# Kernel tuning notes

Measured on AMD Instinct MI355X. Metric: run time of the kernel, lower is better.

The kernel has to match this reference:

```python
import jax, jax.numpy as jnp
import numpy as np

B, N, H, S, NSEC = 1, 8192, 256, 128, 8
TAU = 0.5
DEPTH_LO, DEPTH_HI = 0.0, 2.4
PADDING = 0.1
EPS = 1e-6
_p = float(np.clip(TAU, 1e-4, 1.0 - 1e-4))
LOGIT_TAU = float(np.log(_p / (1.0 - _p)))


def mlp(p, W1, b1, W2, b2, W3, b3, W4, b4):
    # p: [..., 3] -> logit [...]
    h = jax.nn.softplus(p @ W1 + b1)
    h = jax.nn.softplus(h @ W2 + b2)
    h = jax.nn.softplus(h @ W3 + b3)
    return (h @ W4 + b4)[..., 0]


def cube_intersection(ray0, rd):
    # Faithful port of check_ray_intersection_with_unit_cube.
    p_dist = 0.5 + PADDING / 2.0
    plane = jnp.concatenate([jnp.full((3,), p_dist), jnp.full((3,), -p_dist)])  # (6,)
    nom = plane - jnp.tile(ray0, (1, 1, 2))          # (B,N,6)
    den = jnp.tile(rd, (1, 1, 2))
    den = jnp.where(jnp.abs(den) < 1e-9, 1e-9, den)  # numerical guard
    d_int = nom / den                                 # (B,N,6)
    p_int = ray0[:, :, None, :] + d_int[..., None] * rd[:, :, None, :]  # (B,N,6,3)
    inside = jnp.all(jnp.abs(p_int) <= p_dist + EPS, axis=-1)           # (B,N,6)
    mask = inside.sum(-1) == 2                                           # rays hitting cube
    # pick the (exactly two) intersecting planes in ascending plane order,
    # matching torch boolean indexing semantics
    plane_id = jnp.arange(6)
    key = jnp.where(inside, plane_id, plane_id + 6)
    idx2 = jnp.argsort(key, axis=-1)[..., :2]                            # (B,N,2)
    p2 = jnp.take_along_axis(p_int, idx2[..., None], axis=2)            # (B,N,2,3)
    norm_rd = jnp.linalg.norm(rd, axis=-1)                               # (B,N)
    d2 = jnp.linalg.norm(p2 - ray0[:, :, None, :], axis=-1) / norm_rd[..., None]
    d2 = jnp.where(mask[..., None], d2, 0.0)
    d2 = jnp.sort(d2, axis=-1)
    return d2, mask


def _secant(d_low, f_low, d_high, f_high):
    den = f_high - f_low
    den = jnp.where(jnp.abs(den) < 1e-12, 1e-12, den)
    return -f_low * (d_high - d_low) / den + d_low


def reference(ray0, ray_direction, W1, b1, W2, b2, W3, b3, W4, b4):
    rd = ray_direction
    dec = lambda p: mlp(p, W1, b1, W2, b2, W3, b3, W4, b4)
    sg = jax.lax.stop_gradient

    # ---- proposal depths (no grad, as torch no_grad ray-marching) ----
    t = jnp.linspace(0.0, 1.0, S)                       # (S,)
    d_default = DEPTH_LO + t * (DEPTH_HI - DEPTH_LO)
    d2, mask_cube = cube_intersection(ray0, rd)
    d_cube = d2[..., 0:1] + t * (d2[..., 1:2] - d2[..., 0:1])   # (B,N,S)
    d_prop = jnp.where(mask_cube[..., None], d_cube, d_default)
    d_prop = sg(d_prop)

    p_prop = sg(ray0)[:, :, None, :] + d_prop[..., None] * sg(rd)[:, :, None, :]
    val = sg(dec(p_prop)) - LOGIT_TAU                   # (B,N,S)

    mask_0_not_occupied = val[..., 0] < 0
    sign_matrix = jnp.concatenate(
        [jnp.sign(val[..., :-1] * val[..., 1:]), jnp.ones(val.shape[:-1] + (1,), val.dtype)], -1)
    cost = sign_matrix * jnp.arange(S, 0, -1, dtype=val.dtype)
    idx = jnp.argmin(cost, -1)                          # first sign-change step
    vmin = jnp.min(cost, -1)
    f_low = jnp.take_along_axis(val, idx[..., None], -1)[..., 0]
    mask = (vmin < 0) & (f_low < 0) & mask_0_not_occupied

    idx_hi = jnp.minimum(idx + 1, S - 1)
    d_low = jnp.take_along_axis(d_prop, idx[..., None], -1)[..., 0]
    d_high = jnp.take_along_axis(d_prop, idx_hi[..., None], -1)[..., 0]
    f_high = jnp.take_along_axis(val, idx_hi[..., None], -1)[..., 0]

    # ---- secant refinement (no grad in torch) ----
    r0s, rds = sg(ray0), sg(rd)
    d_pred = _secant(d_low, f_low, d_high, f_high)
    for _ in range(NSEC):
        f_mid = sg(dec(r0s + d_pred[..., None] * rds)) - LOGIT_TAU
        low = f_mid < 0
        d_low = jnp.where(low, d_pred, d_low)
        f_low = jnp.where(low, f_mid, f_low)
        d_high = jnp.where(low, d_high, d_pred)
        f_high = jnp.where(low, f_high, f_mid)
        d_pred = _secant(d_low, f_low, d_high, f_high)

    # ---- differentiable implicit-gradient correction (analytic backward of
    # DepthFunction: dd/dtheta = -(df/dtheta)/(df/dd) at the surface point) ----
    d_star = sg(d_pred)
    f_of_d = lambda d: dec(ray0 + d[..., None] * rd) - LOGIT_TAU
    f_val = f_of_d(d_star)                              # differentiable wrt params/rays
    _, df_dd = jax.jvp(f_of_d, (d_star,), (jnp.ones_like(d_star),))
    df_dd = sg(df_dd)
    df_dd = jnp.where(jnp.abs(df_dd) < 1e-6,
                      jnp.where(df_dd < 0, -1e-6, 1e-6), df_dd)
    d_out = d_star - f_val / df_dd
    d_final = jnp.where(mask, d_out, 0.0)
    return d_final


def setup_inputs() -> dict:
    key = jax.random.key(0)
    ks = jax.random.split(key, 10)
    origin = jnp.array([0.0, 0.0, -1.5])
    ray0 = origin + 0.01 * jax.random.normal(ks[0], (B, N, 3), dtype=jnp.float32)
    target = jax.random.uniform(ks[1], (B, N, 3), minval=-0.4, maxval=0.4, dtype=jnp.float32)
    rd = target - ray0
    rd = rd / jnp.linalg.norm(rd, axis=-1, keepdims=True)
    W1 = jax.random.normal(ks[2], (3, H), dtype=jnp.float32) / jnp.sqrt(3.0)
    b1 = 0.1 * jax.random.normal(ks[3], (H,), dtype=jnp.float32)
    W2 = jax.random.normal(ks[4], (H, H), dtype=jnp.float32) / jnp.sqrt(float(H))
    b2 = 0.1 * jax.random.normal(ks[5], (H,), dtype=jnp.float32)
    W3 = jax.random.normal(ks[6], (H, H), dtype=jnp.float32) / jnp.sqrt(float(H))
    b3 = 0.1 * jax.random.normal(ks[7], (H,), dtype=jnp.float32)
    W4 = jax.random.normal(ks[8], (H, 1), dtype=jnp.float32) / jnp.sqrt(float(H))
    b4 = 0.1 * jax.random.normal(ks[9], (1,), dtype=jnp.float32)
    return {"ray0": ray0, "ray_direction": rd, "W1": W1, "b1": b1,
            "W2": W2, "b2": b2, "W3": W3, "b3": b3, "W4": W4, "b4": b4}
```

## Files before the change

kernel.cpp:

```cpp
#include <hip/hip_runtime.h>
#include <math.h>

#define NRAY 8192
#define SSAMP 128
#define HD 256
#define AROW 264
#define A1ROW 40
#define FIXCAP 262144
#define FIXTHR 0.018f

typedef short s16x8 __attribute__((ext_vector_type(8)));
typedef float f32x4 __attribute__((ext_vector_type(4)));

__device__ __forceinline__ unsigned short f2bf(float f) {
    unsigned u = __float_as_uint(f);
    u += 0x7fffu + ((u >> 16) & 1u);
    return (unsigned short)(u >> 16);
}
__device__ __forceinline__ float bf2f(unsigned short s) {
    return __uint_as_float(((unsigned)s) << 16);
}
__device__ __forceinline__ void split2(float f, unsigned short& hi, unsigned short& lo) {
    unsigned u = __float_as_uint(f);
    hi = (unsigned short)(u >> 16);
    float r = f - __uint_as_float(u & 0xFFFF0000u);
    lo = f2bf(r);
}
__device__ __forceinline__ unsigned pack_bf16x2(float a, float b) {
    unsigned r;
    asm("v_cvt_pk_bf16_f32 %0, %1, %2" : "=v"(r) : "v"(a), "v"(b));
    return r;
}
__device__ __forceinline__ float softplus_fast(float x) {
    return fmaxf(x, 0.0f) + __logf(1.0f + __expf(-fabsf(x)));
}
__device__ __forceinline__ float softplus_cheap(float x) {
    float m = __expf(-fabsf(x));
    float p = fmaf(m, fmaf(0.14258f, m, -0.44943f), 1.0f);
    return fmaxf(x, 0.0f) + m * p;
}
__device__ __forceinline__ float sigmoid_fast(float x) {
    return 1.0f / (1.0f + __expf(-x));
}

__global__ __launch_bounds__(256)
void prep_kernel(const float* __restrict__ W1, const float* __restrict__ b1,
                 const float* __restrict__ W2, const float* __restrict__ W3,
                 const float* __restrict__ ray0, const float* __restrict__ rdg,
                 unsigned short* __restrict__ P2, unsigned short* __restrict__ P3,
                 unsigned short* __restrict__ B1, float* __restrict__ rayinfo,
                 int* __restrict__ fix_cnt) {
    const int b = blockIdx.x, tid = threadIdx.x;
    if (b < 256) {
        int idx = b * 256 + tid;
        int k = idx >> 8, n = idx & 255;
        int nt = n >> 4, kt = k >> 5, lq = (k >> 3) & 3, j = k & 7;
        int lane = (lq << 4) | (n & 15);
        size_t off = (size_t)((nt * 8 + kt) * 2) * 512 + (size_t)lane * 8 + j;
        float w = W2[idx];
        unsigned short hi = f2bf(w);
        P2[off] = hi; P2[off + 512] = f2bf(w - bf2f(hi));
        w = W3[idx];
        hi = f2bf(w);
        P3[off] = hi; P3[off + 512] = f2bf(w - bf2f(hi));
    } else if (b < 288) {
        int idx = (b - 256) * 256 + tid;
        int w = idx & 511;
        int lane = w >> 3, j = w & 7;
        int k = ((lane >> 4) << 3) + j;
        int n = ((idx >> 9) << 4) + (lane & 15);
        unsigned short s = 0;
        if (k < 3) s = f2bf(W1[k * HD + n]);
        else if (k == 3) s = f2bf(b1[n]);
        else if (k < 7) s = f2bf(W1[(k - 4) * HD + n]);
        else if (k == 7) { unsigned short bh = f2bf(b1[n]); s = f2bf(b1[n] - bf2f(bh)); }
        else if (k < 11) { float wv = W1[(k - 8) * HD + n]; unsigned short wh = f2bf(wv); s = f2bf(wv - bf2f(wh)); }
        B1[idx] = s;
    } else {
        int r = (b - 288) * 256 + tid;
        if (r == 0) *fix_cnt = 0;
        float o0 = ray0[3 * r], o1 = ray0[3 * r + 1], o2 = ray0[3 * r + 2];
        float v0 = rdg[3 * r], v1 = rdg[3 * r + 1], v2 = rdg[3 * r + 2];
        const float pd = 0.55f, lim = pd + 1e-6f;
        float di[6]; int insk[6]; int cnt = 0;
        for (int k = 0; k < 6; k++) {
            int a = k % 3;
            float pl = (k < 3) ? pd : -pd;
            float den = (a == 0) ? v0 : ((a == 1) ? v1 : v2);
            if (fabsf(den) < 1e-9f) den = 1e-9f;
            float oa = (a == 0) ? o0 : ((a == 1) ? o1 : o2);
            float dd = (pl - oa) / den;
            float px = o0 + dd * v0, py = o1 + dd * v1, pz = o2 + dd * v2;
            int ins = (fabsf(px) <= lim) && (fabsf(py) <= lim) && (fabsf(pz) <= lim);
            di[k] = dd; insk[k] = ins; cnt += ins;
        }
        float d0 = 0.f, sl = 2.4f;
        if (cnt == 2) {
            int k1 = -1, k2 = -1;
            for (int k = 0; k < 6; k++) if (insk[k]) { if (k1 < 0) k1 = k; else k2 = k; }
            float nrd = sqrtf(v0 * v0 + v1 * v1 + v2 * v2);
            float ax = di[k1] * v0, ay = di[k1] * v1, az = di[k1] * v2;
            float d1n = sqrtf(ax * ax + ay * ay + az * az) / nrd;
            float bx = di[k2] * v0, by = di[k2] * v1, bz = di[k2] * v2;
            float d2n = sqrtf(bx * bx + by * by + bz * bz) / nrd;
            d0 = fminf(d1n, d2n);
            sl = fmaxf(d1n, d2n) - d0;
        }
        float* ri = rayinfo + (size_t)r * 8;
        ri[0] = d0; ri[1] = sl;
        ri[2] = o0; ri[3] = o1; ri[4] = o2;
        ri[5] = v0; ri[6] = v1; ri[7] = v2;
    }
}


template<int MT, int NT>
__device__ __forceinline__ void gemm_l1(const unsigned short* A1,
                                        const unsigned short* __restrict__ B1,
                                        f32x4 acc[MT][NT], int lane, int ntbase) {
    const int r15 = lane & 15, q = lane >> 4;
    s16x8 wh[NT];
#pragma unroll
    for (int nt = 0; nt < NT; nt++)
        wh[nt] = *(((const s16x8*)B1) + (size_t)(ntbase + nt) * 64 + lane);
#pragma unroll
    for (int mt = 0; mt < MT; mt++) {
        s16x8 ah = *(const s16x8*)(A1 + (mt * 16 + r15) * A1ROW + q * 8);
#pragma unroll
        for (int nt = 0; nt < NT; nt++)
            acc[mt][nt] = __builtin_amdgcn_mfma_f32_16x16x32_bf16(wh[nt], ah, (f32x4){0.f,0.f,0.f,0.f}, 0, 0, 0);
    }
}

template<int MT, int NT>
__device__ __forceinline__ void gemm_1t(const unsigned short* Act,
                                        const unsigned short* __restrict__ Wp,
                                        f32x4 acc[MT][NT], int lane, int ntbase) {
#pragma unroll
    for (int mt = 0; mt < MT; mt++)
#pragma unroll
        for (int nt = 0; nt < NT; nt++) acc[mt][nt] = (f32x4){0.f, 0.f, 0.f, 0.f};
    const int r15 = lane & 15, q = lane >> 4;
#pragma unroll 2
    for (int kt = 0; kt < 8; kt++) {
        s16x8 wh[NT];
#pragma unroll
        for (int nt = 0; nt < NT; nt++) {
            const s16x8* wp = ((const s16x8*)Wp) + (size_t)((ntbase + nt) * 8 + kt) * 128 + lane;
            wh[nt] = wp[0];
        }
        const int kc = kt * 32 + q * 8;
#pragma unroll
        for (int mt = 0; mt < MT; mt++) {
            s16x8 ah = *(const s16x8*)(Act + (mt * 16 + r15) * AROW + kc);
#pragma unroll
            for (int nt = 0; nt < NT; nt++)
                acc[mt][nt] = __builtin_amdgcn_mfma_f32_16x16x32_bf16(wh[nt], ah, acc[mt][nt], 0, 0, 0);
        }
    }
}

template<int MT, int NT>
__device__ __forceinline__ void gemm_3t(const unsigned short* Ahi, const unsigned short* Alo,
                                        const unsigned short* __restrict__ Wp,
                                        f32x4 acc[MT][NT], int lane, int ntbase) {
#pragma unroll
    for (int mt = 0; mt < MT; mt++)
#pragma unroll
        for (int nt = 0; nt < NT; nt++) acc[mt][nt] = (f32x4){0.f, 0.f, 0.f, 0.f};
    const int r15 = lane & 15, q = lane >> 4;
#pragma unroll 2
    for (int kt = 0; kt < 8; kt++) {
        s16x8 wh[NT], wl[NT];
#pragma unroll
        for (int nt = 0; nt < NT; nt++) {
            const s16x8* wp = ((const s16x8*)Wp) + (size_t)((ntbase + nt) * 8 + kt) * 128 + lane;
            wh[nt] = wp[0];
            wl[nt] = wp[64];
        }
        const int kc = kt * 32 + q * 8;
#pragma unroll
        for (int mt = 0; mt < MT; mt++) {
            s16x8 ah = *(const s16x8*)(Ahi + (mt * 16 + r15) * AROW + kc);
            s16x8 al = *(const s16x8*)(Alo + (mt * 16 + r15) * AROW + kc);
#pragma unroll
            for (int nt = 0; nt < NT; nt++) {
                acc[mt][nt] = __builtin_amdgcn_mfma_f32_16x16x32_bf16(wh[nt], ah, acc[mt][nt], 0, 0, 0);
                acc[mt][nt] = __builtin_amdgcn_mfma_f32_16x16x32_bf16(wl[nt], ah, acc[mt][nt], 0, 0, 0);
                acc[mt][nt] = __builtin_amdgcn_mfma_f32_16x16x32_bf16(wh[nt], al, acc[mt][nt], 0, 0, 0);
            }
        }
    }
}

template<int MT, int NT>
__device__ __forceinline__ void gemm_dual(const unsigned short* Avh, const unsigned short* Avl,
                                          const unsigned short* Ath, const unsigned short* Atl,
                                          const unsigned short* __restrict__ Wp,
                                          f32x4 av[MT][NT], f32x4 at[MT][NT], int lane, int ntbase) {
#pragma unroll
    for (int mt = 0; mt < MT; mt++)
#pragma unroll
        for (int nt = 0; nt < NT; nt++) {
            av[mt][nt] = (f32x4){0.f, 0.f, 0.f, 0.f};
            at[mt][nt] = (f32x4){0.f, 0.f, 0.f, 0.f};
        }
    const int r15 = lane & 15, q = lane >> 4;
#pragma unroll 2
    for (int kt = 0; kt < 8; kt++) {
        s16x8 wh[NT], wl[NT];
#pragma unroll
        for (int nt = 0; nt < NT; nt++) {
            const s16x8* wp = ((const s16x8*)Wp) + (size_t)((ntbase + nt) * 8 + kt) * 128 + lane;
            wh[nt] = wp[0];
            wl[nt] = wp[64];
        }
        const int kc = kt * 32 + q * 8;
#pragma unroll
        for (int mt = 0; mt < MT; mt++) {
            s16x8 avhf = *(const s16x8*)(Avh + (mt * 16 + r15) * AROW + kc);
            s16x8 avlf = *(const s16x8*)(Avl + (mt * 16 + r15) * AROW + kc);
            s16x8 athf = *(const s16x8*)(Ath + (mt * 16 + r15) * AROW + kc);
            s16x8 atlf = *(const s16x8*)(Atl + (mt * 16 + r15) * AROW + kc);
#pragma unroll
            for (int nt = 0; nt < NT; nt++) {
                av[mt][nt] = __builtin_amdgcn_mfma_f32_16x16x32_bf16(wh[nt], avhf, av[mt][nt], 0, 0, 0);
                av[mt][nt] = __builtin_amdgcn_mfma_f32_16x16x32_bf16(wl[nt], avhf, av[mt][nt], 0, 0, 0);
                av[mt][nt] = __builtin_amdgcn_mfma_f32_16x16x32_bf16(wh[nt], avlf, av[mt][nt], 0, 0, 0);
                at[mt][nt] = __builtin_amdgcn_mfma_f32_16x16x32_bf16(wh[nt], athf, at[mt][nt], 0, 0, 0);
                at[mt][nt] = __builtin_amdgcn_mfma_f32_16x16x32_bf16(wl[nt], athf, at[mt][nt], 0, 0, 0);
                at[mt][nt] = __builtin_amdgcn_mfma_f32_16x16x32_bf16(wh[nt], atlf, at[mt][nt], 0, 0, 0);
            }
        }
    }
}

template<int MT, int NT>
__device__ __forceinline__ void epi_l1(f32x4 acc[MT][NT], unsigned short* Ahi, int lane, int wn0) {
    const int r15 = lane & 15, q = lane >> 4;
#pragma unroll
    for (int mt = 0; mt < MT; mt++) {
        unsigned short* rowp = Ahi + (mt * 16 + r15) * AROW + wn0 + q * 4;
#pragma unroll
        for (int nt = 0; nt < NT; nt++) {
            float h0 = softplus_cheap(acc[mt][nt][0]);
            float h1 = softplus_cheap(acc[mt][nt][1]);
            float h2 = softplus_cheap(acc[mt][nt][2]);
            float h3 = softplus_cheap(acc[mt][nt][3]);
            *reinterpret_cast<uint2*>(rowp + nt * 16) =
                make_uint2(pack_bf16x2(h0, h1), pack_bf16x2(h2, h3));
        }
    }
}

template<int MT, int NT>
__device__ __forceinline__ void epi_l1_sp(f32x4 acc[MT][NT], unsigned short* Ahi, unsigned short* Alo,
                                          int lane, int wn0) {
    const int r15 = lane & 15, q = lane >> 4;
#pragma unroll
    for (int mt = 0; mt < MT; mt++) {
        const int rowoff = (mt * 16 + r15) * AROW + wn0 + q * 4;
#pragma unroll
        for (int nt = 0; nt < NT; nt++) {
            float h0 = softplus_fast(acc[mt][nt][0]);
            float h1 = softplus_fast(acc[mt][nt][1]);
            float h2 = softplus_fast(acc[mt][nt][2]);
            float h3 = softplus_fast(acc[mt][nt][3]);
            unsigned x0 = pack_bf16x2(h0, h1), x1 = pack_bf16x2(h2, h3);
            float l0 = h0 - __uint_as_float(x0 << 16);
            float l1 = h1 - __uint_as_float(x0 & 0xFFFF0000u);
            float l2 = h2 - __uint_as_float(x1 << 16);
            float l3 = h3 - __uint_as_float(x1 & 0xFFFF0000u);
            *reinterpret_cast<uint2*>(Ahi + rowoff + nt * 16) = make_uint2(x0, x1);
            *reinterpret_cast<uint2*>(Alo + rowoff + nt * 16) =
                make_uint2(pack_bf16x2(l0, l1), pack_bf16x2(l2, l3));
        }
    }
}

template<int MT, int NT>
__device__ __forceinline__ void epi_hidden_1t(f32x4 acc[MT][NT], const float* __restrict__ b,
                                              unsigned short* Ahi, int lane, int wn0) {
    const int r15 = lane & 15, q = lane >> 4;
    f32x4 bb[NT];
#pragma unroll
    for (int nt = 0; nt < NT; nt++) bb[nt] = *(const f32x4*)(b + wn0 + nt * 16 + q * 4);
#pragma unroll
    for (int mt = 0; mt < MT; mt++) {
        unsigned short* rowp = Ahi + (mt * 16 + r15) * AROW + wn0 + q * 4;
#pragma unroll
        for (int nt = 0; nt < NT; nt++) {
            float h0 = softplus_cheap(acc[mt][nt][0] + bb[nt][0]);
            float h1 = softplus_cheap(acc[mt][nt][1] + bb[nt][1]);
            float h2 = softplus_cheap(acc[mt][nt][2] + bb[nt][2]);
            float h3 = softplus_cheap(acc[mt][nt][3] + bb[nt][3]);
            *reinterpret_cast<uint2*>(rowp + nt * 16) =
                make_uint2(pack_bf16x2(h0, h1), pack_bf16x2(h2, h3));
        }
    }
}

template<int MT, int NT>
__device__ __forceinline__ void epi_hidden_sp(f32x4 acc[MT][NT], const float* __restrict__ b,
                                              unsigned short* Ahi, unsigned short* Alo,
                                              int lane, int wn0) {
    const int r15 = lane & 15, q = lane >> 4;
    f32x4 bb[NT];
#pragma unroll
    for (int nt = 0; nt < NT; nt++) bb[nt] = *(const f32x4*)(b + wn0 + nt * 16 + q * 4);
#pragma unroll
    for (int mt = 0; mt < MT; mt++) {
        const int rowoff = (mt * 16 + r15) * AROW + wn0 + q * 4;
#pragma unroll
        for (int nt = 0; nt < NT; nt++) {
            float h0 = softplus_fast(acc[mt][nt][0] + bb[nt][0]);
            float h1 = softplus_fast(acc[mt][nt][1] + bb[nt][1]);
            float h2 = softplus_fast(acc[mt][nt][2] + bb[nt][2]);
            float h3 = softplus_fast(acc[mt][nt][3] + bb[nt][3]);
            unsigned x0 = pack_bf16x2(h0, h1), x1 = pack_bf16x2(h2, h3);
            float l0 = h0 - __uint_as_float(x0 << 16);
            float l1 = h1 - __uint_as_float(x0 & 0xFFFF0000u);
            float l2 = h2 - __uint_as_float(x1 << 16);
            float l3 = h3 - __uint_as_float(x1 & 0xFFFF0000u);
            *reinterpret_cast<uint2*>(Ahi + rowoff + nt * 16) = make_uint2(x0, x1);
            *reinterpret_cast<uint2*>(Alo + rowoff + nt * 16) =
                make_uint2(pack_bf16x2(l0, l1), pack_bf16x2(l2, l3));
        }
    }
}

template<int MT, int NT>
__device__ __forceinline__ void epi_dual(f32x4 av[MT][NT], f32x4 at[MT][NT], const float* __restrict__ b,
                                         unsigned short* Avh, unsigned short* Avl,
                                         unsigned short* Ath, unsigned short* Atl,
                                         int lane, int wn0) {
    const int r15 = lane & 15, q = lane >> 4;
    f32x4 bb[NT];
#pragma unroll
    for (int nt = 0; nt < NT; nt++) bb[nt] = *(const f32x4*)(b + wn0 + nt * 16 + q * 4);
#pragma unroll
    for (int mt = 0; mt < MT; mt++) {
        const int rowoff = (mt * 16 + r15) * AROW + wn0 + q * 4;
#pragma unroll
        for (int nt = 0; nt < NT; nt++) {
            float h[4], g[4];
#pragma unroll
            for (int r = 0; r < 4; r++) {
                float z = av[mt][nt][r] + bb[nt][r];
                h[r] = softplus_fast(z);
                g[r] = sigmoid_fast(z) * at[mt][nt][r];
            }
            unsigned x0 = pack_bf16x2(h[0], h[1]), x1 = pack_bf16x2(h[2], h[3]);
            float l0 = h[0] - __uint_as_float(x0 << 16);
            float l1 = h[1] - __uint_as_float(x0 & 0xFFFF0000u);
            float l2 = h[2] - __uint_as_float(x1 << 16);
            float l3 = h[3] - __uint_as_float(x1 & 0xFFFF0000u);
            *reinterpret_cast<uint2*>(Avh + rowoff + nt * 16) = make_uint2(x0, x1);
            *reinterpret_cast<uint2*>(Avl + rowoff + nt * 16) =
                make_uint2(pack_bf16x2(l0, l1), pack_bf16x2(l2, l3));
            x0 = pack_bf16x2(g[0], g[1]); x1 = pack_bf16x2(g[2], g[3]);
            l0 = g[0] - __uint_as_float(x0 << 16);
            l1 = g[1] - __uint_as_float(x0 & 0xFFFF0000u);
            l2 = g[2] - __uint_as_float(x1 << 16);
            l3 = g[3] - __uint_as_float(x1 & 0xFFFF0000u);
            *reinterpret_cast<uint2*>(Ath + rowoff + nt * 16) = make_uint2(x0, x1);
            *reinterpret_cast<uint2*>(Atl + rowoff + nt * 16) =
                make_uint2(pack_bf16x2(l0, l1), pack_bf16x2(l2, l3));
        }
    }
}

template<int MT, int NT, bool CH>
__device__ __forceinline__ void l4_reduce(f32x4 acc[MT][NT], const float* __restrict__ b3,
                                          const float* __restrict__ W4,
                                          float* partial, int lane, int wn0) {
    const int r15 = lane & 15, q = lane >> 4;
    f32x4 w4v[NT], b3v[NT];
#pragma unroll
    for (int nt = 0; nt < NT; nt++) {
        w4v[nt] = *(const f32x4*)(W4 + wn0 + nt * 16 + q * 4);
        b3v[nt] = *(const f32x4*)(b3 + wn0 + nt * 16 + q * 4);
    }
#pragma unroll
    for (int mt = 0; mt < MT; mt++) {
        float p = 0.f;
#pragma unroll
        for (int nt = 0; nt < NT; nt++)
#pragma unroll
            for (int r = 0; r < 4; r++) {
                float z = acc[mt][nt][r] + b3v[nt][r];
                float h = CH ? softplus_cheap(z) : softplus_fast(z);
                p = fmaf(h, w4v[nt][r], p);
            }
        p += __shfl_xor(p, 16, 64);
        p += __shfl_xor(p, 32, 64);
        if (q == 0) partial[mt * 16 + r15] = p;
    }
}

template<int MT, int NT>
__device__ __forceinline__ void l4_reduce_dual(f32x4 av[MT][NT], f32x4 at[MT][NT],
                                               const float* __restrict__ b3, const float* __restrict__ W4,
                                               float* pv, float* pt, int lane, int wn0) {
    const int r15 = lane & 15, q = lane >> 4;
    f32x4 w4v[NT], b3v[NT];
#pragma unroll
    for (int nt = 0; nt < NT; nt++) {
        w4v[nt] = *(const f32x4*)(W4 + wn0 + nt * 16 + q * 4);
        b3v[nt] = *(const f32x4*)(b3 + wn0 + nt * 16 + q * 4);
    }
#pragma unroll
    for (int mt = 0; mt < MT; mt++) {
        float sv = 0.f, st = 0.f;
#pragma unroll
        for (int nt = 0; nt < NT; nt++)
#pragma unroll
            for (int r = 0; r < 4; r++) {
                float z = av[mt][nt][r] + b3v[nt][r];
                sv = fmaf(softplus_fast(z), w4v[nt][r], sv);
                st = fmaf(sigmoid_fast(z) * at[mt][nt][r], w4v[nt][r], st);
            }
        sv += __shfl_xor(sv, 16, 64);
        sv += __shfl_xor(sv, 32, 64);
        st += __shfl_xor(st, 16, 64);
        st += __shfl_xor(st, 32, 64);
        if (q == 0) {
            pv[mt * 16 + r15] = sv;
            pt[mt * 16 + r15] = st;
        }
    }
}

__global__ __launch_bounds__(512, 4)
void coarse_mfma(const float* __restrict__ rayinfo,
                 const unsigned short* __restrict__ B1,
                 const unsigned short* __restrict__ P2, const float* __restrict__ b2,
                 const unsigned short* __restrict__ P3, const float* __restrict__ b3,
                 const float* __restrict__ W4, const float* __restrict__ b4,
                 float* __restrict__ val_out, float* __restrict__ dprop_out,
                 int* __restrict__ fix_cnt, int* __restrict__ fix_list) {
    __shared__ __align__(16) unsigned short Ahi[128 * AROW];
    __shared__ __align__(16) unsigned short A1[128 * A1ROW];
    float* partial = (float*)A1;
    const int tid = threadIdx.x;
    const int lane = tid & 63, wave = tid >> 6;
    const int r = blockIdx.x;

    if (tid < 128) {
        const float* ri = rayinfo + (size_t)r * 8;
        const int s = tid;
        float t = (float)s * (1.0f / 127.0f);
        float d = fmaf(t, ri[1], ri[0]);
        dprop_out[r * SSAMP + s] = d;
        float px = fmaf(d, ri[5], ri[2]);
        float py = fmaf(d, ri[6], ri[3]);
        float pz = fmaf(d, ri[7], ri[4]);
        unsigned short hx, lx, hy, ly, hz, lz;
        split2(px, hx, lx); split2(py, hy, ly); split2(pz, hz, lz);
        unsigned short* row = A1 + tid * A1ROW;
        row[0] = hx; row[1] = hy; row[2] = hz; row[3] = 0x3F80u;
        row[4] = lx; row[5] = ly; row[6] = lz; row[7] = 0x3F80u;
        row[8] = hx; row[9] = hy; row[10] = hz;
#pragma unroll
        for (int c = 11; c < 32; c++) row[c] = 0;
    }
    __syncthreads();
    f32x4 acc[8][2];
    gemm_l1<8, 2>(A1, B1, acc, lane, wave * 2);
    epi_l1<8, 2>(acc, Ahi, lane, wave * 32);
    __syncthreads();
    gemm_1t<8, 2>(Ahi, P2, acc, lane, wave * 2);
    __syncthreads();
    epi_hidden_1t<8, 2>(acc, b2, Ahi, lane, wave * 32);
    __syncthreads();
    gemm_1t<8, 2>(Ahi, P3, acc, lane, wave * 2);
    l4_reduce<8, 2, true>(acc, b3, W4, &partial[wave * 128], lane, wave * 32);
    __syncthreads();
    if (tid < 128) {
        float v = b4[0];
#pragma unroll
        for (int w = 0; w < 8; w++) v += partial[w * 128 + tid];
        int idx = r * SSAMP + tid;
        val_out[idx] = v;
        if (fabsf(v) < FIXTHR) {
            int pos = atomicAdd(fix_cnt, 1);
            if (pos < FIXCAP) fix_list[pos] = idx;
        }
    }
}

__global__ __launch_bounds__(256, 4)
void fixup3_mfma(const int* __restrict__ counter, const int* __restrict__ list,
                 float* __restrict__ val, const float* __restrict__ dprop,
                 const float* __restrict__ ray0, const float* __restrict__ rdg,
                 const unsigned short* __restrict__ B1,
                 const unsigned short* __restrict__ P2, const float* __restrict__ b2,
                 const unsigned short* __restrict__ P3, const float* __restrict__ b3,
                 const float* __restrict__ W4, const float* __restrict__ b4) {
    __shared__ __align__(16) unsigned short Ahi[32 * AROW];
    __shared__ __align__(16) unsigned short Alo[32 * AROW];
    __shared__ __align__(16) unsigned short A1[32 * A1ROW];
    __shared__ float partial[4][32];
    __shared__ int bidxs[32];
    const int cnt = min(*counter, FIXCAP);
    const int base = blockIdx.x * 32;
    if (base >= cnt) return;
    const int tid = threadIdx.x;
    const int lane = tid & 63, wave = tid >> 6;
    if (tid < 32) {
        const int i = min(base + tid, cnt - 1);
        const int bidx = list[i];
        bidxs[tid] = bidx;
        const int rr = bidx >> 7;
        float d = dprop[bidx];
        float px = ray0[3 * rr] + d * rdg[3 * rr];
        float py = ray0[3 * rr + 1] + d * rdg[3 * rr + 1];
        float pz = ray0[3 * rr + 2] + d * rdg[3 * rr + 2];
        unsigned short hx, lx, hy, ly, hz, lz;
        split2(px, hx, lx); split2(py, hy, ly); split2(pz, hz, lz);
        unsigned short* row = A1 + tid * A1ROW;
        row[0] = hx; row[1] = hy; row[2] = hz; row[3] = 0x3F80u;
        row[4] = lx; row[5] = ly; row[6] = lz; row[7] = 0x3F80u;
        row[8] = hx; row[9] = hy; row[10] = hz;
#pragma unroll
        for (int c = 11; c < 32; c++) row[c] = 0;
    }
    __syncthreads();
    f32x4 acc[2][4];
    gemm_l1<2, 4>(A1, B1, acc, lane, wave * 4);
    epi_l1_sp<2, 4>(acc, Ahi, Alo, lane, wave * 64);
    __syncthreads();
    gemm_3t<2, 4>(Ahi, Alo, P2, acc, lane, wave * 4);
    __syncthreads();
    epi_hidden_sp<2, 4>(acc, b2, Ahi, Alo, lane, wave * 64);
    __syncthreads();
    gemm_3t<2, 4>(Ahi, Alo, P3, acc, lane, wave * 4);
    l4_reduce<2, 4, false>(acc, b3, W4, &partial[wave][0], lane, wave * 64);
    __syncthreads();
    if (tid < 32) {
        float v = partial[0][tid] + partial[1][tid] + partial[2][tid] + partial[3][tid] + b4[0];
        val[bidxs[tid]] = v;
    }
}

__global__ __launch_bounds__(256, 4)
void refine_mfma(const float* __restrict__ val, const float* __restrict__ dprop,
                 const float* __restrict__ ray0, const float* __restrict__ rdg,
                 const float* __restrict__ W1, const float* __restrict__ b1,
                 const unsigned short* __restrict__ P2, const float* __restrict__ b2,
                 const unsigned short* __restrict__ P3, const float* __restrict__ b3,
                 const float* __restrict__ W4, const float* __restrict__ b4,
                 float* __restrict__ out) {
    __shared__ __align__(16) unsigned short Avh[16 * AROW];
    __shared__ __align__(16) unsigned short Avl[16 * AROW];
    __shared__ __align__(16) unsigned short Ath[16 * AROW];
    __shared__ __align__(16) unsigned short Atl[16 * AROW];
    __shared__ float partial[4][16], ptan[4][16];
    __shared__ float dl[16], fl[16], dh[16], fh[16], dps[16];
    __shared__ int mks[16];
    unsigned short* Ahi = Avh;
    const int tid = threadIdx.x;
    const int lane = tid & 63, wave = tid >> 6;
    const int r0 = blockIdx.x * 16;

    for (int i = 0; i < 4; i++) {
        const int r = r0 + wave * 4 + i;
        const float2 v = *(const float2*)(val + (size_t)r * SSAMP + lane * 2);
        const float2 dd = *(const float2*)(dprop + (size_t)r * SSAMP + lane * 2);
        float vnext = __shfl_down(v.x, 1, 64);
        const int s0 = lane * 2, s1 = s0 + 1;
        float pr0 = v.x * v.y;
        int sg0 = (pr0 > 0.f) ? 1 : ((pr0 < 0.f) ? -1 : 0);
        int k0 = (sg0 * (SSAMP - s0) + 129) * 256 + s0;
        int k1;
        if (lane == 63) {
            k1 = (1 + 129) * 256 + 127;
        } else {
            float pr1 = v.y * vnext;
            int sg1 = (pr1 > 0.f) ? 1 : ((pr1 < 0.f) ? -1 : 0);
            k1 = (sg1 * (SSAMP - s1) + 129) * 256 + s1;
        }
        int k = min(k0, k1);
#pragma unroll
        for (int m = 1; m < 64; m <<= 1) k = min(k, __shfl_xor(k, m, 64));
        int bidx = k & 255;
        int cmin = (k >> 8) - 129;
        int idxh = min(bidx + 1, SSAMP - 1);
        int ow = bidx >> 1, oh = idxh >> 1;
        float fa = __shfl(v.x, ow, 64), fb = __shfl(v.y, ow, 64);
        float da = __shfl(dd.x, ow, 64), db = __shfl(dd.y, ow, 64);
        float fa2 = __shfl(v.x, oh, 64), fb2 = __shfl(v.y, oh, 64);
        float da2 = __shfl(dd.x, oh, 64), db2 = __shfl(dd.y, oh, 64);
        float v0 = __shfl(v.x, 0, 64);
        if (lane == 0) {
            float f_low = (bidx & 1) ? fb : fa;
            float d_low = (bidx & 1) ? db : da;
            float f_high = (idxh & 1) ? fb2 : fa2;
            float d_high = (idxh & 1) ? db2 : da2;
            int sl = wave * 4 + i;
            mks[sl] = (cmin < 0) && (f_low < 0.f) && (v0 < 0.f);
            float den = f_high - f_low;
            if (fabsf(den) < 1e-12f) den = 1e-12f;
            dl[sl] = d_low; fl[sl] = f_low; dh[sl] = d_high; fh[sl] = f_high;
            dps[sl] = -f_low * (d_high - d_low) / den + d_low;
        }
    }
    __syncthreads();
    for (int it = 0; it < 8; it++) {
        {
            const int pt = tid >> 4, jb = (tid & 15) << 4;
            const int rr = r0 + pt;
            float d = dps[pt];
            float px = ray0[3 * rr] + d * rdg[3 * rr];
            float py = ray0[3 * rr + 1] + d * rdg[3 * rr + 1];
            float pz = ray0[3 * rr + 2] + d * rdg[3 * rr + 2];
            for (int j = jb; j < jb + 16; j += 4) {
                float4 wa = *(const float4*)(W1 + j);
                float4 wb = *(const float4*)(W1 + 256 + j);
                float4 wc = *(const float4*)(W1 + 512 + j);
                float4 bb = *(const float4*)(b1 + j);
                float z[4];
                z[0] = fmaf(px, wa.x, fmaf(py, wb.x, fmaf(pz, wc.x, bb.x)));
                z[1] = fmaf(px, wa.y, fmaf(py, wb.y, fmaf(pz, wc.y, bb.y)));
                z[2] = fmaf(px, wa.z, fmaf(py, wb.z, fmaf(pz, wc.z, bb.z)));
                z[3] = fmaf(px, wa.w, fmaf(py, wb.w, fmaf(pz, wc.w, bb.w)));
                *reinterpret_cast<uint2*>(&Ahi[pt * AROW + j]) =
                    make_uint2(pack_bf16x2(softplus_cheap(z[0]), softplus_cheap(z[1])),
                               pack_bf16x2(softplus_cheap(z[2]), softplus_cheap(z[3])));
            }
        }
        __syncthreads();
        f32x4 acc[1][4];
        gemm_1t<1, 4>(Ahi, P2, acc, lane, wave * 4);
        __syncthreads();
        epi_hidden_1t<1, 4>(acc, b2, Ahi, lane, wave * 64);
        __syncthreads();
        gemm_1t<1, 4>(Ahi, P3, acc, lane, wave * 4);
        l4_reduce<1, 4, true>(acc, b3, W4, &partial[wave][0], lane, wave * 64);
        __syncthreads();
        if (tid < 16) {
            float fm = partial[0][tid] + partial[1][tid] + partial[2][tid] + partial[3][tid] + b4[0];
            float dpv = dps[tid];
            float dlv = dl[tid], flv = fl[tid], dhv = dh[tid], fhv = fh[tid];
            if (fm < 0.f) { dlv = dpv; flv = fm; } else { dhv = dpv; fhv = fm; }
            float den = fhv - flv;
            if (fabsf(den) < 1e-12f) den = 1e-12f;
            dps[tid] = -flv * (dhv - dlv) / den + dlv;
            dl[tid] = dlv; fl[tid] = flv; dh[tid] = dhv; fh[tid] = fhv;
        }
        __syncthreads();
    }
    {
        const int pt = tid >> 4, jb = (tid & 15) << 4;
        const int rr = r0 + pt;
        float d = dps[pt];
        float v0 = rdg[3 * rr], v1 = rdg[3 * rr + 1], v2 = rdg[3 * rr + 2];
        float px = ray0[3 * rr] + d * v0;
        float py = ray0[3 * rr + 1] + d * v1;
        float pz = ray0[3 * rr + 2] + d * v2;
        for (int j = jb; j < jb + 16; j += 4) {
            float4 wa = *(const float4*)(W1 + j);
            float4 wb = *(const float4*)(W1 + 256 + j);
            float4 wc = *(const float4*)(W1 + 512 + j);
            float4 bb = *(const float4*)(b1 + j);
            float z[4], zt[4], h[4], g[4];
            z[0] = fmaf(px, wa.x, fmaf(py, wb.x, fmaf(pz, wc.x, bb.x)));
            z[1] = fmaf(px, wa.y, fmaf(py, wb.y, fmaf(pz, wc.y, bb.y)));
            z[2] = fmaf(px, wa.z, fmaf(py, wb.z, fmaf(pz, wc.z, bb.z)));
            z[3] = fmaf(px, wa.w, fmaf(py, wb.w, fmaf(pz, wc.w, bb.w)));
            zt[0] = fmaf(v0, wa.x, fmaf(v1, wb.x, v2 * wc.x));
            zt[1] = fmaf(v0, wa.y, fmaf(v1, wb.y, v2 * wc.y));
            zt[2] = fmaf(v0, wa.z, fmaf(v1, wb.z, v2 * wc.z));
            zt[3] = fmaf(v0, wa.w, fmaf(v1, wb.w, v2 * wc.w));
#pragma unroll
            for (int i = 0; i < 4; i++) {
                h[i] = softplus_fast(z[i]);
                g[i] = sigmoid_fast(z[i]) * zt[i];
            }
            unsigned x0 = pack_bf16x2(h[0], h[1]), x1 = pack_bf16x2(h[2], h[3]);
            float l0 = h[0] - __uint_as_float(x0 << 16);
            float l1 = h[1] - __uint_as_float(x0 & 0xFFFF0000u);
            float l2 = h[2] - __uint_as_float(x1 << 16);
            float l3 = h[3] - __uint_as_float(x1 & 0xFFFF0000u);
            *reinterpret_cast<uint2*>(&Avh[pt * AROW + j]) = make_uint2(x0, x1);
            *reinterpret_cast<uint2*>(&Avl[pt * AROW + j]) =
                make_uint2(pack_bf16x2(l0, l1), pack_bf16x2(l2, l3));
            x0 = pack_bf16x2(g[0], g[1]); x1 = pack_bf16x2(g[2], g[3]);
            l0 = g[0] - __uint_as_float(x0 << 16);
            l1 = g[1] - __uint_as_float(x0 & 0xFFFF0000u);
            l2 = g[2] - __uint_as_float(x1 << 16);
            l3 = g[3] - __uint_as_float(x1 & 0xFFFF0000u);
            *reinterpret_cast<uint2*>(&Ath[pt * AROW + j]) = make_uint2(x0, x1);
            *reinterpret_cast<uint2*>(&Atl[pt * AROW + j]) =
                make_uint2(pack_bf16x2(l0, l1), pack_bf16x2(l2, l3));
        }
    }
    __syncthreads();
    f32x4 av[1][4], at[1][4];
    gemm_dual<1, 4>(Avh, Avl, Ath, Atl, P2, av, at, lane, wave * 4);
    __syncthreads();
    epi_dual<1, 4>(av, at, b2, Avh, Avl, Ath, Atl, lane, wave * 64);
    __syncthreads();
    gemm_dual<1, 4>(Avh, Avl, Ath, Atl, P3, av, at, lane, wave * 4);
    l4_reduce_dual<1, 4>(av, at, b3, W4, &partial[wave][0], &ptan[wave][0], lane, wave * 64);
    __syncthreads();
    if (tid < 16) {
        float f = partial[0][tid] + partial[1][tid] + partial[2][tid] + partial[3][tid] + b4[0];
        float ft = ptan[0][tid] + ptan[1][tid] + ptan[2][tid] + ptan[3][tid];
        if (fabsf(ft) < 1e-6f) ft = (ft < 0.f) ? -1e-6f : 1e-6f;
        float dres = dps[tid] - f / ft;
        out[r0 + tid] = mks[tid] ? dres : 0.0f;
    }
}

extern "C" void kernel_launch(void* const* d_in, const int* in_sizes, int n_in,
                              void* d_out, int out_size, void* d_ws, size_t ws_size,
                              hipStream_t stream) {
    const float* ray0 = (const float*)d_in[0];
    const float* rdg  = (const float*)d_in[1];
    const float* W1 = (const float*)d_in[2];
    const float* b1 = (const float*)d_in[3];
    const float* W2 = (const float*)d_in[4];
    const float* b2 = (const float*)d_in[5];
    const float* W3 = (const float*)d_in[6];
    const float* b3 = (const float*)d_in[7];
    const float* W4 = (const float*)d_in[8];
    const float* b4 = (const float*)d_in[9];
    float* out = (float*)d_out;

    float* ws = (float*)d_ws;
    float* val    = ws;
    float* dprop  = ws + (size_t)SSAMP * NRAY;
    unsigned short* P2 = (unsigned short*)(ws + (size_t)2 * SSAMP * NRAY);
    unsigned short* P3 = P2 + 131072;
    unsigned short* B1 = P3 + 131072;
    float* rayinfo = (float*)(B1 + 8192);
    int* fix_cnt  = (int*)(rayinfo + (size_t)NRAY * 8);
    int* fix_list = fix_cnt + 64;

    hipLaunchKernelGGL(prep_kernel, dim3(320), dim3(256), 0, stream,
                       W1, b1, W2, W3, ray0, rdg, P2, P3, B1, rayinfo, fix_cnt);
    hipLaunchKernelGGL(coarse_mfma, dim3(NRAY), dim3(512), 0, stream,
                       rayinfo, B1, P2, b2, P3, b3, W4, b4, val, dprop, fix_cnt, fix_list);
    hipLaunchKernelGGL(fixup3_mfma, dim3(FIXCAP / 32), dim3(256), 0, stream,
                       fix_cnt, fix_list, val, dprop, ray0, rdg,
                       B1, P2, b2, P3, b3, W4, b4);
    hipLaunchKernelGGL(refine_mfma, dim3(NRAY / 16), dim3(256), 0, stream,
                       val, dprop, ray0, rdg, W1, b1, P2, b2, P3, b3, W4, b4, out);
}
```

Before: 689.2 us.

## Keep coarse MLP activations in registers, computing layer 1 on scalar ALUs

The coarse kernel drops its LDS activation tiles. Each wave now owns 16 samples across the full 256-wide hidden dimension, so activations stay in registers and are moved into MFMA operand layout with cross-lane shuffles instead of LDS round trips and block barriers. Layer 1 is computed directly from fp32 W1 with FMAs rather than through a bf16 MFMA. This trades LDS traffic and syncs for much higher register pressure (launch bounds lowered to 2 blocks per CU) and more repeated global or L2 weight loads per wave.

```diff
diff --git a/kernel.cpp b/kernel.cpp
--- a/kernel.cpp
+++ b/kernel.cpp
@@ -113,7 +113,6 @@
     }
 }
 
-
 template<int MT, int NT>
 __device__ __forceinline__ void gemm_l1(const unsigned short* A1,
                                         const unsigned short* __restrict__ B1,
@@ -231,24 +230,6 @@
                 at[mt][nt] = __builtin_amdgcn_mfma_f32_16x16x32_bf16(wl[nt], athf, at[mt][nt], 0, 0, 0);
                 at[mt][nt] = __builtin_amdgcn_mfma_f32_16x16x32_bf16(wh[nt], atlf, at[mt][nt], 0, 0, 0);
             }
-        }
-    }
-}
-
-template<int MT, int NT>
-__device__ __forceinline__ void epi_l1(f32x4 acc[MT][NT], unsigned short* Ahi, int lane, int wn0) {
-    const int r15 = lane & 15, q = lane >> 4;
-#pragma unroll
-    for (int mt = 0; mt < MT; mt++) {
-        unsigned short* rowp = Ahi + (mt * 16 + r15) * AROW + wn0 + q * 4;
-#pragma unroll
-        for (int nt = 0; nt < NT; nt++) {
-            float h0 = softplus_cheap(acc[mt][nt][0]);
-            float h1 = softplus_cheap(acc[mt][nt][1]);
-            float h2 = softplus_cheap(acc[mt][nt][2]);
-            float h3 = softplus_cheap(acc[mt][nt][3]);
-            *reinterpret_cast<uint2*>(rowp + nt * 16) =
-                make_uint2(pack_bf16x2(h0, h1), pack_bf16x2(h2, h3));
         }
     }
 }
@@ -431,56 +412,110 @@
     }
 }
 
-__global__ __launch_bounds__(512, 4)
+__global__ __launch_bounds__(512, 2)
 void coarse_mfma(const float* __restrict__ rayinfo,
-                 const unsigned short* __restrict__ B1,
+                 const float* __restrict__ W1, const float* __restrict__ b1,
                  const unsigned short* __restrict__ P2, const float* __restrict__ b2,
                  const unsigned short* __restrict__ P3, const float* __restrict__ b3,
                  const float* __restrict__ W4, const float* __restrict__ b4,
                  float* __restrict__ val_out, float* __restrict__ dprop_out,
                  int* __restrict__ fix_cnt, int* __restrict__ fix_list) {
-    __shared__ __align__(16) unsigned short Ahi[128 * AROW];
-    __shared__ __align__(16) unsigned short A1[128 * A1ROW];
-    float* partial = (float*)A1;
     const int tid = threadIdx.x;
     const int lane = tid & 63, wave = tid >> 6;
+    const int q = lane >> 4, r15 = lane & 15;
     const int r = blockIdx.x;
-
-    if (tid < 128) {
-        const float* ri = rayinfo + (size_t)r * 8;
-        const int s = tid;
-        float t = (float)s * (1.0f / 127.0f);
-        float d = fmaf(t, ri[1], ri[0]);
-        dprop_out[r * SSAMP + s] = d;
-        float px = fmaf(d, ri[5], ri[2]);
-        float py = fmaf(d, ri[6], ri[3]);
-        float pz = fmaf(d, ri[7], ri[4]);
-        unsigned short hx, lx, hy, ly, hz, lz;
-        split2(px, hx, lx); split2(py, hy, ly); split2(pz, hz, lz);
-        unsigned short* row = A1 + tid * A1ROW;
-        row[0] = hx; row[1] = hy; row[2] = hz; row[3] = 0x3F80u;
-        row[4] = lx; row[5] = ly; row[6] = lz; row[7] = 0x3F80u;
-        row[8] = hx; row[9] = hy; row[10] = hz;
-#pragma unroll
-        for (int c = 11; c < 32; c++) row[c] = 0;
-    }
-    __syncthreads();
-    f32x4 acc[8][2];
-    gemm_l1<8, 2>(A1, B1, acc, lane, wave * 2);
-    epi_l1<8, 2>(acc, Ahi, lane, wave * 32);
-    __syncthreads();
-    gemm_1t<8, 2>(Ahi, P2, acc, lane, wave * 2);
-    __syncthreads();
-    epi_hidden_1t<8, 2>(acc, b2, Ahi, lane, wave * 32);
-    __syncthreads();
-    gemm_1t<8, 2>(Ahi, P3, acc, lane, wave * 2);
-    l4_reduce<8, 2, true>(acc, b3, W4, &partial[wave * 128], lane, wave * 32);
-    __syncthreads();
-    if (tid < 128) {
-        float v = b4[0];
-#pragma unroll
-        for (int w = 0; w < 8; w++) v += partial[w * 128 + tid];
-        int idx = r * SSAMP + tid;
+    const int s = wave * 16 + r15;
+
+    const float* ri = rayinfo + (size_t)r * 8;
+    const float t = (float)s * (1.0f / 127.0f);
+    const float d = fmaf(t, ri[1], ri[0]);
+    const float px = fmaf(d, ri[5], ri[2]);
+    const float py = fmaf(d, ri[6], ri[3]);
+    const float pz = fmaf(d, ri[7], ri[4]);
+    if (q == 0) dprop_out[r * SSAMP + s] = d;
+
+    unsigned pk[16][2];
+    const int c0 = q * 4;
+#pragma unroll
+    for (int nt = 0; nt < 16; nt++) {
+        const int c = nt * 16 + c0;
+        float4 wa = *(const float4*)(W1 + c);
+        float4 wb = *(const float4*)(W1 + 256 + c);
+        float4 wc = *(const float4*)(W1 + 512 + c);
+        float4 bb = *(const float4*)(b1 + c);
+        float z0 = fmaf(px, wa.x, fmaf(py, wb.x, fmaf(pz, wc.x, bb.x)));
+        float z1 = fmaf(px, wa.y, fmaf(py, wb.y, fmaf(pz, wc.y, bb.y)));
+        float z2 = fmaf(px, wa.z, fmaf(py, wb.z, fmaf(pz, wc.z, bb.z)));
+        float z3 = fmaf(px, wa.w, fmaf(py, wb.w, fmaf(pz, wc.w, bb.w)));
+        pk[nt][0] = pack_bf16x2(softplus_cheap(z0), softplus_cheap(z1));
+        pk[nt][1] = pack_bf16x2(softplus_cheap(z2), softplus_cheap(z3));
+    }
+
+    const int srcA = ((q & 1) << 5) | r15;
+    const int srcB = srcA + 16;
+    const int hiSel = q >> 1;
+
+    f32x4 acc[16];
+
+#define COARSE_LAYER(WP)                                                              \
+    {                                                                                 \
+        const s16x8* WV = (const s16x8*)(WP);                                         \
+        _Pragma("unroll")                                                             \
+        for (int nt = 0; nt < 16; nt++) acc[nt] = (f32x4){0.f, 0.f, 0.f, 0.f};        \
+        _Pragma("unroll")                                                             \
+        for (int kt = 0; kt < 8; kt++) {                                              \
+            s16x8 w[16];                                                              \
+            _Pragma("unroll")                                                         \
+            for (int nt = 0; nt < 16; nt++)                                           \
+                w[nt] = WV[(size_t)(nt * 8 + kt) * 128 + lane];                       \
+            unsigned lo0 = __shfl(pk[2 * kt][0], srcA, 64);                           \
+            unsigned hi0 = __shfl(pk[2 * kt + 1][0], srcA, 64);                       \
+            unsigned lo1 = __shfl(pk[2 * kt][1], srcA, 64);                           \
+            unsigned hi1 = __shfl(pk[2 * kt + 1][1], srcA, 64);                       \
+            unsigned w0 = hiSel ? hi0 : lo0;                                          \
+            unsigned w1 = hiSel ? hi1 : lo1;                                          \
+            lo0 = __shfl(pk[2 * kt][0], srcB, 64);                                    \
+            hi0 = __shfl(pk[2 * kt + 1][0], srcB, 64);                                \
+            lo1 = __shfl(pk[2 * kt][1], srcB, 64);                                    \
+            hi1 = __shfl(pk[2 * kt + 1][1], srcB, 64);                                \
+            unsigned w2 = hiSel ? hi0 : lo0;                                          \
+            unsigned w3 = hiSel ? hi1 : lo1;                                          \
+            union { unsigned u[4]; s16x8 v; } bu;                                     \
+            bu.u[0] = w0; bu.u[1] = w1; bu.u[2] = w2; bu.u[3] = w3;                   \
+            const s16x8 bf = bu.v;                                                    \
+            __builtin_amdgcn_s_barrier();  \
+            _Pragma("unroll")                                                         \
+            for (int nt = 0; nt < 16; nt++)                                           \
+                acc[nt] = __builtin_amdgcn_mfma_f32_16x16x32_bf16(w[nt], bf, acc[nt], 0, 0, 0); \
+        }                                                                             \
+    }
+
+    COARSE_LAYER(P2);
+#pragma unroll
+    for (int nt = 0; nt < 16; nt++) {
+        float4 bb = *(const float4*)(b2 + nt * 16 + c0);
+        pk[nt][0] = pack_bf16x2(softplus_cheap(acc[nt][0] + bb.x), softplus_cheap(acc[nt][1] + bb.y));
+        pk[nt][1] = pack_bf16x2(softplus_cheap(acc[nt][2] + bb.z), softplus_cheap(acc[nt][3] + bb.w));
+    }
+
+    COARSE_LAYER(P3);
+#undef COARSE_LAYER
+
+    float p = 0.f;
+#pragma unroll
+    for (int nt = 0; nt < 16; nt++) {
+        float4 bb = *(const float4*)(b3 + nt * 16 + c0);
+        float4 ww = *(const float4*)(W4 + nt * 16 + c0);
+        p = fmaf(softplus_cheap(acc[nt][0] + bb.x), ww.x, p);
+        p = fmaf(softplus_cheap(acc[nt][1] + bb.y), ww.y, p);
+        p = fmaf(softplus_cheap(acc[nt][2] + bb.z), ww.z, p);
+        p = fmaf(softplus_cheap(acc[nt][3] + bb.w), ww.w, p);
+    }
+    p += __shfl_xor(p, 16, 64);
+    p += __shfl_xor(p, 32, 64);
+    if (q == 0) {
+        float v = p + b4[0];
+        int idx = r * SSAMP + s;
         val_out[idx] = v;
         if (fabsf(v) < FIXTHR) {
             int pos = atomicAdd(fix_cnt, 1);
@@ -741,7 +776,7 @@
     hipLaunchKernelGGL(prep_kernel, dim3(320), dim3(256), 0, stream,
                        W1, b1, W2, W3, ray0, rdg, P2, P3, B1, rayinfo, fix_cnt);
     hipLaunchKernelGGL(coarse_mfma, dim3(NRAY), dim3(512), 0, stream,
-                       rayinfo, B1, P2, b2, P3, b3, W4, b4, val, dprop, fix_cnt, fix_list);
+                       rayinfo, W1, b1, P2, b2, P3, b3, W4, b4, val, dprop, fix_cnt, fix_list);
     hipLaunchKernelGGL(fixup3_mfma, dim3(FIXCAP / 32), dim3(256), 0, stream,
                        fix_cnt, fix_list, val, dprop, ray0, rdg,
                        B1, P2, b2, P3, b3, W4, b4);
```

New measurement: 1.185 ms. 1.72x slower.
